# Performance work log

Measured on AMD Instinct MI355X. Metric: run time of the kernel, lower is better.

The kernel has to match this reference:

```python
import jax, jax.numpy as jnp
import numpy as np

N_SUPPORT = 4096
N_QUERY = 8192
H = W = 28
IN_DIM = H * W  # 784
EMBED_DIM = 512
N_CLASSES = 64


def setup_inputs() -> dict:
    key = jax.random.key(0)
    k1, k2, k3, k4 = jax.random.split(key, 4)
    support_set = jax.random.normal(k1, (N_SUPPORT, 1, H, W), dtype=jnp.float32)
    query_set = jax.random.normal(k2, (N_QUERY, 1, H, W), dtype=jnp.float32)
    # one-hot support labels (N, C)
    lbl = jax.random.randint(k3, (N_SUPPORT,), 0, N_CLASSES)
    support_labels = jax.nn.one_hot(lbl, N_CLASSES, dtype=jnp.float32)
    # encoder params: flatten + dense projection stand-in for embedding_net
    W_enc = jax.random.normal(k4, (IN_DIM, EMBED_DIM), dtype=jnp.float32) * (1.0 / np.sqrt(IN_DIM))
    b_enc = jnp.zeros((EMBED_DIM,), dtype=jnp.float32)
    return {
        "support_set": support_set,
        "query_set": query_set,
        "support_labels": support_labels,
        "W_enc": W_enc,
        "b_enc": b_enc,
    }


def _encode(x, W_enc, b_enc):
    # (B, 1, H, W) -> (B, D): flatten + linear projection
    B = x.shape[0]
    return x.reshape(B, -1) @ W_enc + b_enc


def _neg_cdist(q, s):
    # -euclidean distance, computed via the expansion ||q-s||^2 = |q|^2 + |s|^2 - 2 q.s
    q2 = jnp.sum(q * q, axis=-1, keepdims=True)          # (Q, 1)
    s2 = jnp.sum(s * s, axis=-1)[None, :]                # (1, N)
    qs = jnp.einsum("qd,nd->qn", q, s)                  # (Q, N)
    d2 = jnp.maximum(q2 + s2 - 2.0 * qs, 0.0)
    return -jnp.sqrt(d2)


def reference(support_set, query_set, support_labels, W_enc, b_enc):
    support_emb = _encode(support_set, W_enc, b_enc)     # (N, D)
    query_emb = _encode(query_set, W_enc, b_enc)         # (Q, D)
    distances = _neg_cdist(query_emb, support_emb)       # (Q, N)
    attention = jax.nn.softmax(distances, axis=1)        # (Q, N)
    predictions = attention @ support_labels             # (Q, C)
    return predictions
```

## Files before the change

kernel.cpp:

```cpp
#include <hip/hip_runtime.h>

#define N_SUP 4096
#define N_QRY 8192
#define IN_DIM 784
#define EMB 512
#define NCLS 64
#define M_TOT (N_SUP + N_QRY)
#define NCHUNK 25
#define XCH 13

typedef _Float16 f16;
typedef _Float16 f16x8 __attribute__((ext_vector_type(8)));
typedef float f32x4 __attribute__((ext_vector_type(4)));

#define GLDS16(gp, lp)                                                        \
    __builtin_amdgcn_global_load_lds(                                         \
        (const __attribute__((address_space(1))) void*)(gp),                  \
        (__attribute__((address_space(3))) void*)(lp), 16, 0, 0)

static __device__ __forceinline__ f16x8 cvt8(const float* p) {
    float4 a = *(const float4*)p;
    float4 b = *(const float4*)(p + 4);
    f16x8 v;
    v[0] = (f16)a.x; v[1] = (f16)a.y; v[2] = (f16)a.z; v[3] = (f16)a.w;
    v[4] = (f16)b.x; v[5] = (f16)b.y; v[6] = (f16)b.z; v[7] = (f16)b.w;
    return v;
}

__global__ __launch_bounds__(256) void prep_wb(const float* __restrict__ W,
                                               f16* __restrict__ Wb) {
    int g = blockIdx.x * 256 + threadIdx.x;
    if (g >= NCHUNK * 32 * 64) return;
    int chunk = g >> 11;
    int rem = g & 2047;
    int nbg = rem >> 6, lane = rem & 63;
    int n = nbg * 16 + (lane & 15);
    int kbase = chunk * 32 + (lane >> 4) * 8;
    f16x8 v;
#pragma unroll
    for (int j = 0; j < 8; ++j) {
        int k = kbase + j;
        v[j] = (k < IN_DIM) ? (f16)W[(size_t)k * EMB + n] : (f16)0.f;
    }
    *(f16x8*)(Wb + (size_t)g * 8) = v;
}

__global__ __launch_bounds__(256) void prep_lbl(const float* __restrict__ lab,
                                                int* __restrict__ lbl) {
    const int w = threadIdx.x >> 6, lane = threadIdx.x & 63;
    const int s = blockIdx.x * 4 + w;
    float v = lab[(size_t)s * NCLS + lane];
    int c = lane;
#pragma unroll
    for (int off = 1; off < 64; off <<= 1) {
        float v2 = __shfl_xor(v, off);
        int c2 = __shfl_xor(c, off);
        if (v2 > v || (v2 == v && c2 < c)) { v = v2; c = c2; }
    }
    if (lane == 0) lbl[s] = c;
}

__global__ __launch_bounds__(256) void prep_L(const int* __restrict__ lbl,
                                              f16* __restrict__ Lcs) {
    int idx = blockIdx.x * 256 + threadIdx.x;
    if (idx >= NCLS * N_SUP) return;
    int c = idx >> 12, s = idx & (N_SUP - 1);
    Lcs[idx] = (lbl[s] == c) ? (f16)1.f : (f16)0.f;
}

__global__ __launch_bounds__(256) void prep_sb(const f16* __restrict__ E,
                                               f16* __restrict__ Sb) {
    int g = blockIdx.x * 256 + threadIdx.x;
    int s = g >> 6, lg = g & 63;
    f16x8 v = *(const f16x8*)(E + (size_t)s * EMB + lg * 8);
    *(f16x8*)(Sb + (size_t)s * EMB + ((lg ^ (s & 15)) * 8)) = v;
}

__global__ __launch_bounds__(256) void encode(
    const float* __restrict__ sup, const float* __restrict__ qry,
    const f16* __restrict__ Wb, const float* __restrict__ bias,
    f16* __restrict__ E, float* __restrict__ norms)
{
    __shared__ __align__(16) f16 Xs[32][72];
    const int tid = threadIdx.x;
    const int w = tid >> 6, lane = tid & 63;
    const int q = lane >> 4, c16 = lane & 15;
    const int mb = blockIdx.x >> 1;
    const int ch = blockIdx.x & 1;
    const int m0 = mb * 32;
    const int rbase = (w & 1) * 16;
    const int nbg0 = ch * 16 + (w >> 1) * 8;
    const int cbase = nbg0 * 16;

    f32x4 acc[8];
#pragma unroll
    for (int nb = 0; nb < 8; ++nb) acc[nb] = (f32x4){0.f, 0.f, 0.f, 0.f};

    const int sr = tid >> 3;
    const int sq = tid & 7;
    const float* xrow;
    {
        int gr = m0 + sr;
        xrow = (gr < N_SUP) ? sup + (size_t)gr * IN_DIM
                            : qry + (size_t)(gr - N_SUP) * IN_DIM;
    }

    f16x8 xg = cvt8(xrow + sq * 8);

    for (int c = 0; c < XCH; ++c) {
        __syncthreads();
        *(f16x8*)&Xs[sr][sq * 8] = xg;
        __syncthreads();
        if (c + 1 < XCH) {
            int k = (c + 1) * 64 + sq * 8;
            xg = (k + 8 <= IN_DIM) ? cvt8(xrow + k) : (f16x8){0,0,0,0,0,0,0,0};
        }
#pragma unroll
        for (int kc = 0; kc < 2; ++kc) {
            int c32 = c * 2 + kc;
            if (c32 >= NCHUNK) break;
            f16x8 a = *(const f16x8*)&Xs[rbase + c16][kc * 32 + q * 8];
            const f16* wb = Wb + ((size_t)(c32 * 32 + nbg0) * 64 + lane) * 8;
#pragma unroll
            for (int nb = 0; nb < 8; ++nb) {
                f16x8 b = *(const f16x8*)(wb + (size_t)nb * 512);
                acc[nb] = __builtin_amdgcn_mfma_f32_16x16x32_f16(a, b, acc[nb], 0, 0, 0);
            }
        }
    }

    float nrm[4] = {0.f, 0.f, 0.f, 0.f};
#pragma unroll
    for (int nb = 0; nb < 8; ++nb) {
        int col = cbase + nb * 16 + c16;
        float bv = bias[col];
#pragma unroll
        for (int r = 0; r < 4; ++r) {
            int row = m0 + rbase + q * 4 + r;
            float v = acc[nb][r] + bv;
            E[(size_t)row * EMB + col] = (f16)v;
            nrm[r] += v * v;
        }
    }
#pragma unroll
    for (int r = 0; r < 4; ++r) {
        float v = nrm[r];
        v += __shfl_xor(v, 1); v += __shfl_xor(v, 2);
        v += __shfl_xor(v, 4); v += __shfl_xor(v, 8);
        if (c16 == 0) atomicAdd(&norms[m0 + rbase + q * 4 + r], v);
    }
}

__global__ __launch_bounds__(256) void anchor(const f16* __restrict__ E,
                                              const float* __restrict__ norms,
                                              float* __restrict__ manc) {
    const int w = threadIdx.x >> 6, lane = threadIdx.x & 63;
    const int qrow = blockIdx.x * 4 + w;
    f16x8 qv = *(const f16x8*)(E + (size_t)(N_SUP + qrow) * EMB + lane * 8);
    f16x8 sv = *(const f16x8*)(E + lane * 8);
    float dot = 0.f;
#pragma unroll
    for (int j = 0; j < 8; ++j) dot += (float)qv[j] * (float)sv[j];
    dot += __shfl_xor(dot, 1);  dot += __shfl_xor(dot, 2);
    dot += __shfl_xor(dot, 4);  dot += __shfl_xor(dot, 8);
    dot += __shfl_xor(dot, 16); dot += __shfl_xor(dot, 32);
    if (lane == 0) {
        float d2 = fmaxf(norms[N_SUP + qrow] + norms[0] - 2.f * dot, 0.f);
        manc[qrow] = sqrtf(d2);
    }
}

__global__ __launch_bounds__(256, 2) void attn(
    const f16* __restrict__ E, const float* __restrict__ norms,
    const float* __restrict__ manc, const f16* __restrict__ Lcs,
    const f16* __restrict__ Sb, float* __restrict__ Num)
{
    __shared__ __align__(16) f16 Ss[2][32 * EMB];
    __shared__ __align__(16) f16 Pt[4][16][40];
    const int tid = threadIdx.x;
    const int w = tid >> 6, lane = tid & 63;
    const int q = lane >> 4, c16 = lane & 15;
    const int ss = blockIdx.x & 7;
    const int qt = blockIdx.x >> 3;

    f16x8 qf[16];
    const f16* qb = E + (size_t)(N_SUP + qt * 64 + w * 16 + c16) * EMB + q * 8;
#pragma unroll
    for (int ks = 0; ks < 16; ++ks) qf[ks] = *(const f16x8*)(qb + ks * 32);
    float q2[4], mrow[4];
#pragma unroll
    for (int r = 0; r < 4; ++r) {
        q2[r]   = norms[N_SUP + qt * 64 + w * 16 + q * 4 + r];
        mrow[r] = manc[qt * 64 + w * 16 + q * 4 + r];
    }

    f32x4 accPL[4];
#pragma unroll
    for (int nb = 0; nb < 4; ++nb) accPL[nb] = (f32x4){0.f, 0.f, 0.f, 0.f};

    const f16* sb_base = Sb + (size_t)(ss * 512) * EMB;
    const int wslot = w * 512;

#pragma unroll
    for (int i = 0; i < 8; ++i)
        GLDS16(sb_base + (size_t)(wslot + i * 64 + lane) * 8,
               &Ss[0][(wslot + i * 64) * 8]);
    __syncthreads();

    for (int t = 0; t < 16; ++t) {
        const int cur = t & 1;
        if (t + 1 < 16) {
            const f16* gsrc = sb_base + (size_t)(t + 1) * 32 * EMB;
#pragma unroll
            for (int i = 0; i < 8; ++i)
                GLDS16(gsrc + (size_t)(wslot + i * 64 + lane) * 8,
                       &Ss[cur ^ 1][(wslot + i * 64) * 8]);
        }
        const int s0g = ss * 512 + t * 32;
        f16x8 bl[4];
#pragma unroll
        for (int nbc = 0; nbc < 4; ++nbc)
            bl[nbc] = *(const f16x8*)(Lcs + (size_t)(nbc * 16 + c16) * N_SUP + s0g + q * 8);

        f32x4 accQK[2];
        accQK[0] = (f32x4){0.f, 0.f, 0.f, 0.f};
        accQK[1] = (f32x4){0.f, 0.f, 0.f, 0.f};
#pragma unroll
        for (int kc = 0; kc < 4; ++kc) {
#pragma unroll
            for (int ksl = 0; ksl < 4; ++ksl) {
                const int lg = kc * 16 + ksl * 4 + q;
#pragma unroll
                for (int nb = 0; nb < 2; ++nb) {
                    const int r = nb * 16 + c16;
                    f16x8 b = *(const f16x8*)&Ss[cur][r * EMB + ((lg ^ c16) * 8)];
                    accQK[nb] = __builtin_amdgcn_mfma_f32_16x16x32_f16(
                        qf[kc * 4 + ksl], b, accQK[nb], 0, 0, 0);
                }
            }
        }
#pragma unroll
        for (int nb = 0; nb < 2; ++nb) {
            const int col = s0g + nb * 16 + c16;
            const float s2 = norms[col];
#pragma unroll
            for (int r = 0; r < 4; ++r) {
                float d2 = fmaxf(q2[r] + s2 - 2.f * accQK[nb][r], 0.f);
                float p = __expf(mrow[r] - sqrtf(d2));
                p = fminf(p, 60000.f);
                Pt[w][q * 4 + r][nb * 16 + c16] = (f16)p;
            }
        }
        f16x8 af = *(const f16x8*)&Pt[w][c16][q * 8];
#pragma unroll
        for (int nbc = 0; nbc < 4; ++nbc)
            accPL[nbc] = __builtin_amdgcn_mfma_f32_16x16x32_f16(af, bl[nbc], accPL[nbc], 0, 0, 0);

        __syncthreads();
    }

#pragma unroll
    for (int nbc = 0; nbc < 4; ++nbc)
#pragma unroll
        for (int r = 0; r < 4; ++r)
            atomicAdd(&Num[(size_t)(qt * 64 + w * 16 + q * 4 + r) * NCLS + nbc * 16 + c16],
                      accPL[nbc][r]);
}

__global__ __launch_bounds__(256) void finalize(const float* __restrict__ Num,
                                                float* __restrict__ out) {
    const int tid = threadIdx.x;
    const int w = tid >> 6, lane = tid & 63;
    const int qrow = blockIdx.x * 4 + w;
    float v = Num[(size_t)qrow * NCLS + lane];
    float s = v;
    s += __shfl_xor(s, 1);  s += __shfl_xor(s, 2);  s += __shfl_xor(s, 4);
    s += __shfl_xor(s, 8);  s += __shfl_xor(s, 16); s += __shfl_xor(s, 32);
    out[(size_t)qrow * NCLS + lane] = v / s;
}

extern "C" void kernel_launch(void* const* d_in, const int* in_sizes, int n_in,
                              void* d_out, int out_size, void* d_ws, size_t ws_size,
                              hipStream_t stream) {
    (void)in_sizes; (void)n_in; (void)out_size; (void)ws_size;
    const float* sup  = (const float*)d_in[0];
    const float* qry  = (const float*)d_in[1];
    const float* lab  = (const float*)d_in[2];
    const float* Wenc = (const float*)d_in[3];
    const float* benc = (const float*)d_in[4];
    float* out = (float*)d_out;

    char* ws = (char*)d_ws;
    size_t off = 0;
    f16* Wb = (f16*)(ws + off);        off += (size_t)NCHUNK * 32 * 64 * 8 * 2;
    f16* E  = (f16*)(ws + off);        off += (size_t)M_TOT * EMB * 2;
    f16* Sb = (f16*)(ws + off);        off += (size_t)N_SUP * EMB * 2;
    int* lbl = (int*)(ws + off);       off += (size_t)N_SUP * 4;
    f16* Lcs = (f16*)(ws + off);       off += (size_t)NCLS * N_SUP * 2;
    float* manc = (float*)(ws + off);  off += (size_t)N_QRY * 4;
    float* norms = (float*)(ws + off); off += (size_t)M_TOT * 4;
    float* Num = (float*)(ws + off);   off += (size_t)N_QRY * NCLS * 4;

    hipMemsetAsync(norms, 0, (size_t)M_TOT * 4 + (size_t)N_QRY * NCLS * 4, stream);

    prep_wb<<<(NCHUNK * 32 * 64 + 255) / 256, 256, 0, stream>>>(Wenc, Wb);
    prep_lbl<<<N_SUP / 4, 256, 0, stream>>>(lab, lbl);
    prep_L<<<NCLS * N_SUP / 256, 256, 0, stream>>>(lbl, Lcs);
    encode<<<M_TOT / 32 * 2, 256, 0, stream>>>(sup, qry, Wb, benc, E, norms);
    prep_sb<<<N_SUP * 64 / 256, 256, 0, stream>>>(E, Sb);
    anchor<<<N_QRY / 4, 256, 0, stream>>>(E, norms, manc);
    attn<<<N_QRY / 64 * 8, 256, 0, stream>>>(E, norms, manc, Lcs, Sb, Num);
    finalize<<<N_QRY / 4, 256, 0, stream>>>(Num, out);
}
```

Baseline: 199.0 us.

## Halve attn support tile to 16 rows for four blocks per CU

Shrinks the double-buffered support tile in LDS from 32 to 16 rows per step and doubles the loop count, so launch bounds can be raised from two to four blocks per CU. The P·L MFMA and label loads now run every other step, and support norms are staged once in shared memory. It also swaps sqrtf for the hardware sqrt builtin. The cost is twice as many barriers and async-load rounds per block, plus tighter register limits that could cause spilling of the 16 query fragments.

```diff
diff --git a/kernel.cpp b/kernel.cpp
--- a/kernel.cpp
+++ b/kernel.cpp
@@ -170,19 +170,23 @@
     }
 }
 
-__global__ __launch_bounds__(256, 2) void attn(
+__global__ __launch_bounds__(256, 4) void attn(
     const f16* __restrict__ E, const float* __restrict__ norms,
     const float* __restrict__ manc, const f16* __restrict__ Lcs,
     const f16* __restrict__ Sb, float* __restrict__ Num)
 {
-    __shared__ __align__(16) f16 Ss[2][32 * EMB];
+    __shared__ __align__(16) f16 Ss[2][16 * EMB];
     __shared__ __align__(16) f16 Pt[4][16][40];
+    __shared__ float Sn[512];
     const int tid = threadIdx.x;
     const int w = tid >> 6, lane = tid & 63;
     const int q = lane >> 4, c16 = lane & 15;
     const int ss = blockIdx.x & 7;
     const int qt = blockIdx.x >> 3;
 
+    Sn[tid]       = norms[ss * 512 + tid];
+    Sn[256 + tid] = norms[ss * 512 + 256 + tid];
+
     f16x8 qf[16];
     const f16* qb = E + (size_t)(N_SUP + qt * 64 + w * 16 + c16) * EMB + q * 8;
 #pragma unroll
@@ -199,62 +203,60 @@
     for (int nb = 0; nb < 4; ++nb) accPL[nb] = (f32x4){0.f, 0.f, 0.f, 0.f};
 
     const f16* sb_base = Sb + (size_t)(ss * 512) * EMB;
-    const int wslot = w * 512;
-
-#pragma unroll
-    for (int i = 0; i < 8; ++i)
+    const int wslot = w * 256;
+
+#pragma unroll
+    for (int i = 0; i < 4; ++i)
         GLDS16(sb_base + (size_t)(wslot + i * 64 + lane) * 8,
                &Ss[0][(wslot + i * 64) * 8]);
     __syncthreads();
 
-    for (int t = 0; t < 16; ++t) {
+#pragma unroll 2
+    for (int t = 0; t < 32; ++t) {
         const int cur = t & 1;
-        if (t + 1 < 16) {
-            const f16* gsrc = sb_base + (size_t)(t + 1) * 32 * EMB;
-#pragma unroll
-            for (int i = 0; i < 8; ++i)
+        if (t + 1 < 32) {
+            const f16* gsrc = sb_base + (size_t)(t + 1) * 16 * EMB;
+#pragma unroll
+            for (int i = 0; i < 4; ++i)
                 GLDS16(gsrc + (size_t)(wslot + i * 64 + lane) * 8,
                        &Ss[cur ^ 1][(wslot + i * 64) * 8]);
         }
-        const int s0g = ss * 512 + t * 32;
         f16x8 bl[4];
-#pragma unroll
-        for (int nbc = 0; nbc < 4; ++nbc)
-            bl[nbc] = *(const f16x8*)(Lcs + (size_t)(nbc * 16 + c16) * N_SUP + s0g + q * 8);
-
-        f32x4 accQK[2];
-        accQK[0] = (f32x4){0.f, 0.f, 0.f, 0.f};
-        accQK[1] = (f32x4){0.f, 0.f, 0.f, 0.f};
+        if (t & 1) {
+            const int ps0 = ss * 512 + (t >> 1) * 32;
+#pragma unroll
+            for (int nbc = 0; nbc < 4; ++nbc)
+                bl[nbc] = *(const f16x8*)(Lcs + (size_t)(nbc * 16 + c16) * N_SUP + ps0 + q * 8);
+        }
+
+        f32x4 accQK = (f32x4){0.f, 0.f, 0.f, 0.f};
 #pragma unroll
         for (int kc = 0; kc < 4; ++kc) {
 #pragma unroll
             for (int ksl = 0; ksl < 4; ++ksl) {
                 const int lg = kc * 16 + ksl * 4 + q;
-#pragma unroll
-                for (int nb = 0; nb < 2; ++nb) {
-                    const int r = nb * 16 + c16;
-                    f16x8 b = *(const f16x8*)&Ss[cur][r * EMB + ((lg ^ c16) * 8)];
-                    accQK[nb] = __builtin_amdgcn_mfma_f32_16x16x32_f16(
-                        qf[kc * 4 + ksl], b, accQK[nb], 0, 0, 0);
-                }
+                f16x8 b = *(const f16x8*)&Ss[cur][c16 * EMB + ((lg ^ c16) * 8)];
+                accQK = __builtin_amdgcn_mfma_f32_16x16x32_f16(
+                    qf[kc * 4 + ksl], b, accQK, 0, 0, 0);
             }
         }
-#pragma unroll
-        for (int nb = 0; nb < 2; ++nb) {
-            const int col = s0g + nb * 16 + c16;
-            const float s2 = norms[col];
+        {
+            const float s2 = Sn[t * 16 + c16];
+            const int pcol = (t & 1) * 16 + c16;
 #pragma unroll
             for (int r = 0; r < 4; ++r) {
-                float d2 = fmaxf(q2[r] + s2 - 2.f * accQK[nb][r], 0.f);
-                float p = __expf(mrow[r] - sqrtf(d2));
+                float d2 = fmaxf(q2[r] + s2 - 2.f * accQK[r], 0.f);
+                float p = __expf(mrow[r] - __builtin_amdgcn_sqrtf(d2));
                 p = fminf(p, 60000.f);
-                Pt[w][q * 4 + r][nb * 16 + c16] = (f16)p;
+                Pt[w][q * 4 + r][pcol] = (f16)p;
             }
         }
-        f16x8 af = *(const f16x8*)&Pt[w][c16][q * 8];
-#pragma unroll
-        for (int nbc = 0; nbc < 4; ++nbc)
-            accPL[nbc] = __builtin_amdgcn_mfma_f32_16x16x32_f16(af, bl[nbc], accPL[nbc], 0, 0, 0);
+        if (t & 1) {
+            f16x8 af = *(const f16x8*)&Pt[w][c16][q * 8];
+#pragma unroll
+            for (int nbc = 0; nbc < 4; ++nbc)
+                accPL[nbc] = __builtin_amdgcn_mfma_f32_16x16x32_f16(af, bl[nbc], accPL[nbc], 0, 0, 0);
+        }
 
         __syncthreads();
     }
```

Result: slower. 217.5 us (+9.3%).
